# Performance work log

Hardware: AMD Instinct MI355X
Metric: run time of the kernel (lower is better)

## Reference

```python
import jax, jax.numpy as jnp
import numpy as np

N0, N1, N2 = 200000, 50000, 10000
E1, E2 = 800000, 160000
IN_F, HID, RANK, OUT_C = 128, 128, 64, 64


def _cp_graphconv(feat_src, feat_dst, src, dst, n_dst, W_src, W_dst, W_out, b):
    # CP-rank factorized GraphConv: project src feats to rank space, gather along
    # edges, mean-aggregate per dst node, multiply elementwise with dst rank
    # projection (CP / Hadamard fusion), then project to output space.
    h_src = feat_src @ W_src                      # [N_src, R]
    msg = h_src[src]                              # [E, R] gather
    agg = jax.ops.segment_sum(msg, dst, num_segments=n_dst)   # [n_dst, R]
    cnt = jax.ops.segment_sum(jnp.ones((dst.shape[0],), msg.dtype), dst, num_segments=n_dst)
    agg = agg / jnp.maximum(cnt, 1.0)[:, None]    # mean aggregation
    z = agg * (feat_dst @ W_dst)                  # [n_dst, R] CP hadamard
    return z @ W_out + b                          # [n_dst, out]


def setup_inputs() -> dict:
    key = jax.random.key(0)
    ks = jax.random.split(key, 12)
    s1 = 1.0 / np.sqrt(IN_F)
    s2 = 1.0 / np.sqrt(HID)
    sr = 1.0 / np.sqrt(RANK)
    return {
        "x": jax.random.normal(ks[0], (N0, IN_F), jnp.float32),
        "W_src1": jax.random.normal(ks[1], (IN_F, RANK), jnp.float32) * s1,
        "W_dst1": jax.random.normal(ks[2], (IN_F, RANK), jnp.float32) * s1,
        "W_out1": jax.random.normal(ks[3], (RANK, HID), jnp.float32) * sr,
        "b1": jnp.zeros((HID,), jnp.float32),
        "W_src2": jax.random.normal(ks[4], (HID, RANK), jnp.float32) * s2,
        "W_dst2": jax.random.normal(ks[5], (HID, RANK), jnp.float32) * s2,
        "W_out2": jax.random.normal(ks[6], (RANK, OUT_C), jnp.float32) * sr,
        "b2": jnp.zeros((OUT_C,), jnp.float32),
        "src1": jax.random.randint(ks[7], (E1,), 0, N0),
        "dst1": jax.random.randint(ks[8], (E1,), 0, N1),
        "src2": jax.random.randint(ks[9], (E2,), 0, N1),
        "dst2": jax.random.randint(ks[10], (E2,), 0, N2),
        "n_dst1": N1,
        "n_dst2": N2,
    }


def reference(x, W_src1, W_dst1, W_out1, b1, W_src2, W_dst2, W_out2, b2,
              src1, dst1, src2, dst2, n_dst1, n_dst2):
    h_dst = x[:n_dst1]
    h = _cp_graphconv(x, h_dst, src1, dst1, n_dst1, W_src1, W_dst1, W_out1, b1)
    h = jax.nn.relu(h)
    # dropout: eval mode (training=False) -> identity
    h_dst2 = h[:n_dst2]
    out = _cp_graphconv(h, h_dst2, src2, dst2, n_dst2, W_src2, W_dst2, W_out2, b2)
    return out
```

## Files before the change

kernel.cpp:

```cpp
#include <hip/hip_runtime.h>
#include <hip/hip_bf16.h>
#include <hip/hip_fp16.h>

#define N0 200000
#define N1 50000
#define N2 10000
#define E1C 800000
#define E2C 160000
#define NB1 784
#define NB2 160
#define NBT (NB1 + NB2)
#define CH1 64
#define CH2 16
#define NTP 12500
#define NT1 3125
#define NT2 625
#define SCAP 2048

struct H8 { __half2 a, b, c, d; };

typedef _Float16 f16x8 __attribute__((ext_vector_type(8)));
typedef float f32x4 __attribute__((ext_vector_type(4)));
#define MFMA16(a, b, c) __builtin_amdgcn_mfma_f32_16x16x32_f16(a, b, c, 0, 0, 0)

#define WT_TOTAL 45056

__global__ __launch_bounds__(256) void prep_count(const int* __restrict__ dst1,
                                                  const int* __restrict__ dst2,
                                                  int* __restrict__ hist_part,
                                                  const float* __restrict__ Wsrc1,
                                                  const float* __restrict__ Wdst1,
                                                  const float* __restrict__ Wout1,
                                                  const float* __restrict__ Wsrc2,
                                                  const float* __restrict__ Wdst2,
                                                  const float* __restrict__ Wout2,
                                                  __half* __restrict__ wt) {
    int b = blockIdx.x;
    if (b < CH1 + CH2) {
        __shared__ int hl[NB1];
        const int* dst; int nb, e0, n4, hoff;
        if (b < CH1) {
            dst = dst1; nb = NB1; int per = E1C / CH1 / 4; e0 = b * per; n4 = per;
            hoff = b * NB1;
        } else {
            dst = dst2; nb = NB2; int per = E2C / CH2 / 4; int c = b - CH1;
            e0 = c * per; n4 = per;
            hoff = CH1 * NB1 + c * NB2;
        }
        for (int i = threadIdx.x; i < nb; i += 256) hl[i] = 0;
        __syncthreads();
        const int4* d4 = reinterpret_cast<const int4*>(dst);
        for (int i = e0 + threadIdx.x; i < e0 + n4; i += 256) {
            int4 v = d4[i];
            atomicAdd(&hl[v.x >> 6], 1);
            atomicAdd(&hl[v.y >> 6], 1);
            atomicAdd(&hl[v.z >> 6], 1);
            atomicAdd(&hl[v.w >> 6], 1);
        }
        __syncthreads();
        for (int i = threadIdx.x; i < nb; i += 256) hist_part[hoff + i] = hl[i];
    } else {
        int e = (b - (CH1 + CH2)) * 256 + threadIdx.x;
        if (e < WT_TOTAL) {
            float v;
            if (e < 8192)       { int e2 = e;         int n = e2 >> 7, k = e2 & 127; v = Wsrc1[k * 64 + n]; }
            else if (e < 16384) { int e2 = e - 8192;  int n = e2 >> 7, k = e2 & 127; v = Wdst1[k * 64 + n]; }
            else if (e < 24576) { int e2 = e - 16384; int n = e2 >> 6, k = e2 & 63;  v = Wout1[k * 128 + n]; }
            else if (e < 32768) { int e2 = e - 24576; int n = e2 >> 7, k = e2 & 127; v = Wsrc2[k * 64 + n]; }
            else if (e < 40960) { int e2 = e - 32768; int n = e2 >> 7, k = e2 & 127; v = Wdst2[k * 64 + n]; }
            else                { int e2 = e - 40960; int n = e2 >> 6, k = e2 & 63;  v = Wout2[k * 64 + n]; }
            wt[e] = __float2half(v);
        }
    }
}

__global__ __launch_bounds__(1024) void scan_sum(const int* __restrict__ hp,
                                                 int* __restrict__ hist,
                                                 int* __restrict__ base,
                                                 int* __restrict__ cursor) {
    int t = threadIdx.x, lane = t & 63, wid = t >> 6;
    int v = 0;
    if (t < NB1) {
        #pragma unroll 8
        for (int c = 0; c < CH1; ++c) v += hp[c * NB1 + t];
    } else if (t < NBT) {
        const int* hp2 = hp + CH1 * NB1;
        int j = t - NB1;
        #pragma unroll
        for (int c = 0; c < CH2; ++c) v += hp2[c * NB2 + j];
    }
    if (t < NBT) hist[t] = v;
    int s = v;
    #pragma unroll
    for (int o = 1; o < 64; o <<= 1) { int u = __shfl_up(s, o, 64); if (lane >= o) s += u; }
    __shared__ int ws[16];
    if (lane == 63) ws[wid] = s;
    __syncthreads();
    if (wid == 0 && lane < 16) {
        int w = ws[lane];
        #pragma unroll
        for (int o = 1; o < 16; o <<= 1) { int u = __shfl_up(w, o, 64); if (lane >= o) w += u; }
        ws[lane] = w;
    }
    __syncthreads();
    int excl = ((wid == 0) ? 0 : ws[wid - 1]) + (s - v);
    if (t < NBT) { base[t] = excl; cursor[t] = excl; }
}

__global__ __launch_bounds__(256) void sort_scatter(const int* __restrict__ dst1,
                                                    const int* __restrict__ src1,
                                                    const int* __restrict__ dst2,
                                                    const int* __restrict__ src2,
                                                    int* __restrict__ cursor,
                                                    int* __restrict__ edgebuf) {
    __shared__ int cnt_l[98], lbase[98], rsv[98], lcur[98];
    __shared__ int slot[SCAP];
    __shared__ int stot[2];
    int b = blockIdx.x;
    const int* dst; const int* srcp; int goff, bpp, lo, e0, e1;
    if (b < 8 * CH1) {
        dst = dst1; srcp = src1; goff = 0; bpp = NB1 / 8;
        int part = b & 7, chunk = b >> 3;
        lo = part * bpp;
        int per = E1C / CH1 / 4;
        e0 = chunk * per; e1 = e0 + per;
    } else {
        int k = b - 8 * CH1;
        dst = dst2; srcp = src2; goff = NB1; bpp = NB2 / 8;
        int part = k & 7, chunk = k >> 3;
        lo = part * bpp;
        int per = E2C / CH2 / 4;
        e0 = chunk * per; e1 = e0 + per;
    }
    int t = threadIdx.x;
    for (int i = t; i < bpp; i += 256) { cnt_l[i] = 0; lcur[i] = 0; }
    __syncthreads();
    const int4* d4 = reinterpret_cast<const int4*>(dst);
    const int4* s4 = reinterpret_cast<const int4*>(srcp);
    for (int i = e0 + t; i < e1; i += 256) {
        int4 v = d4[i];
        int b0 = (v.x >> 6) - lo; if ((unsigned)b0 < (unsigned)bpp) atomicAdd(&cnt_l[b0], 1);
        int b1 = (v.y >> 6) - lo; if ((unsigned)b1 < (unsigned)bpp) atomicAdd(&cnt_l[b1], 1);
        int b2 = (v.z >> 6) - lo; if ((unsigned)b2 < (unsigned)bpp) atomicAdd(&cnt_l[b2], 1);
        int b3 = (v.w >> 6) - lo; if ((unsigned)b3 < (unsigned)bpp) atomicAdd(&cnt_l[b3], 1);
    }
    __syncthreads();
    if (t < 128) {
        int j = t;
        int lane6 = t & 63;
        int v = (j < bpp) ? cnt_l[j] : 0;
        int s = v;
        #pragma unroll
        for (int o = 1; o < 64; o <<= 1) { int u = __shfl_up(s, o, 64); if (lane6 >= o) s += u; }
        if (lane6 == 63) stot[t >> 6] = s;
        if (j < bpp) lbase[j] = s - v;
    }
    __syncthreads();
    if (t >= 64 && t < 128) {
        int j = t;
        if (j < bpp) lbase[j] += stot[0];
    }
    __syncthreads();
    int T = stot[0] + stot[1];
    if (T <= SCAP) {
        for (int i = e0 + t; i < e1; i += 256) {
            int4 dv = d4[i];
            int4 sv = s4[i];
            int b0 = (dv.x >> 6) - lo;
            if ((unsigned)b0 < (unsigned)bpp) { int p = atomicAdd(&lcur[b0], 1); slot[lbase[b0] + p] = (b0 << 24) | (sv.x << 6) | (dv.x & 63); }
            int b1 = (dv.y >> 6) - lo;
            if ((unsigned)b1 < (unsigned)bpp) { int p = atomicAdd(&lcur[b1], 1); slot[lbase[b1] + p] = (b1 << 24) | (sv.y << 6) | (dv.y & 63); }
            int b2 = (dv.z >> 6) - lo;
            if ((unsigned)b2 < (unsigned)bpp) { int p = atomicAdd(&lcur[b2], 1); slot[lbase[b2] + p] = (b2 << 24) | (sv.z << 6) | (dv.z & 63); }
            int b3 = (dv.w >> 6) - lo;
            if ((unsigned)b3 < (unsigned)bpp) { int p = atomicAdd(&lcur[b3], 1); slot[lbase[b3] + p] = (b3 << 24) | (sv.w << 6) | (dv.w & 63); }
        }
        if (t < bpp) rsv[t] = cnt_l[t] ? atomicAdd(&cursor[goff + lo + t], cnt_l[t]) : 0;
        __syncthreads();
        for (int u = t; u < T; u += 256) {
            int w = slot[u];
            int bx = (unsigned)w >> 24;
            edgebuf[rsv[bx] + (u - lbase[bx])] = w & 0x00FFFFFF;
        }
    } else {
        if (t < bpp) rsv[t] = cnt_l[t] ? atomicAdd(&cursor[goff + lo + t], cnt_l[t]) : 0;
        __syncthreads();
        for (int i = e0 + t; i < e1; i += 256) {
            int4 dv = d4[i];
            int4 sv = s4[i];
            int b0 = (dv.x >> 6) - lo;
            if ((unsigned)b0 < (unsigned)bpp) { int p = atomicAdd(&lcur[b0], 1); edgebuf[rsv[b0] + p] = (sv.x << 6) | (dv.x & 63); }
            int b1 = (dv.y >> 6) - lo;
            if ((unsigned)b1 < (unsigned)bpp) { int p = atomicAdd(&lcur[b1], 1); edgebuf[rsv[b1] + p] = (sv.y << 6) | (dv.y & 63); }
            int b2 = (dv.z >> 6) - lo;
            if ((unsigned)b2 < (unsigned)bpp) { int p = atomicAdd(&lcur[b2], 1); edgebuf[rsv[b2] + p] = (sv.z << 6) | (dv.z & 63); }
            int b3 = (dv.w >> 6) - lo;
            if ((unsigned)b3 < (unsigned)bpp) { int p = atomicAdd(&lcur[b3], 1); edgebuf[rsv[b3] + p] = (sv.w << 6) | (dv.w & 63); }
        }
    }
}

__global__ __launch_bounds__(256) void proj1(const float* __restrict__ x,
                                             const __half* __restrict__ wth,
                                             __half* __restrict__ hsrc,
                                             __half* __restrict__ hdst) {
    int wave = threadIdx.x >> 6, lane = threadIdx.x & 63;
    int tile = blockIdx.x * 4 + wave;
    if (tile >= NTP) return;
    int r0 = tile * 16;
    int m = lane & 15, q = lane >> 4;
    const float* A = x + (size_t)(r0 + m) * 128 + q * 8;
    const _Float16* wt = (const _Float16*)wth;
    const _Float16* Wsrc = wt;
    const _Float16* Wdst = wt + 8192;

    f16x8 a[4];
    #pragma unroll
    for (int kc = 0; kc < 4; ++kc) {
        float4 v0 = *(const float4*)(A + kc * 32);
        float4 v1 = *(const float4*)(A + kc * 32 + 4);
        f16x8 tv;
        tv[0] = (_Float16)v0.x; tv[1] = (_Float16)v0.y; tv[2] = (_Float16)v0.z; tv[3] = (_Float16)v0.w;
        tv[4] = (_Float16)v1.x; tv[5] = (_Float16)v1.y; tv[6] = (_Float16)v1.z; tv[7] = (_Float16)v1.w;
        a[kc] = tv;
    }
    f32x4 accS[4];
    #pragma unroll
    for (int nt = 0; nt < 4; ++nt) accS[nt] = (f32x4)(0.0f);
    #pragma unroll
    for (int kc = 0; kc < 4; ++kc)
        #pragma unroll
        for (int nt = 0; nt < 4; ++nt) {
            f16x8 bb = *(const f16x8*)(Wsrc + (nt * 16 + m) * 128 + kc * 32 + q * 8);
            accS[nt] = MFMA16(a[kc], bb, accS[nt]);
        }
    #pragma unroll
    for (int nt = 0; nt < 4; ++nt)
        #pragma unroll
        for (int i = 0; i < 4; ++i)
            hsrc[(size_t)(r0 + q * 4 + i) * 64 + nt * 16 + m] = __float2half(accS[nt][i]);

    if (tile < NT1) {
        f32x4 accD[4];
        #pragma unroll
        for (int nt = 0; nt < 4; ++nt) accD[nt] = (f32x4)(0.0f);
        #pragma unroll
        for (int kc = 0; kc < 4; ++kc)
            #pragma unroll
            for (int nt = 0; nt < 4; ++nt) {
                f16x8 bb = *(const f16x8*)(Wdst + (nt * 16 + m) * 128 + kc * 32 + q * 8);
                accD[nt] = MFMA16(a[kc], bb, accD[nt]);
            }
        #pragma unroll
        for (int nt = 0; nt < 4; ++nt)
            #pragma unroll
            for (int i = 0; i < 4; ++i)
                hdst[(size_t)(r0 + q * 4 + i) * 64 + nt * 16 + m] = __float2half(accD[nt][i]);
    }
}

__global__ __launch_bounds__(256) void seg1l1(const __half* __restrict__ X,
                                              const __half* __restrict__ hdst1,
                                              const int* __restrict__ edgebuf,
                                              const int* __restrict__ base,
                                              const int* __restrict__ hist,
                                              const __half* __restrict__ wth,
                                              const float* __restrict__ b1,
                                              __half* __restrict__ hsrc2,
                                              __half* __restrict__ hdst2) {
    __shared__ int cnt_lds[64];
    __shared__ int ell[64 * 64];
    __shared__ _Float16 agg[64][72];
    __shared__ _Float16 zt[4][16][136];
    int bkt = blockIdx.x;
    int ebase = base[bkt];
    int ecnt = hist[bkt];
    if (threadIdx.x < 64) cnt_lds[threadIdx.x] = 0;
    __syncthreads();
    for (int i = threadIdx.x; i < ecnt; i += 256) {
        int v = edgebuf[ebase + i];
        int ld = v & 63;
        int p = atomicAdd(&cnt_lds[ld], 1);
        if (p < 64) ell[(ld << 6) + p] = v >> 6;
    }
    __syncthreads();
    int wid = threadIdx.x >> 6, lane = threadIdx.x & 63;
    int sub = lane >> 3, fq = lane & 7;
    const H8* Xr = reinterpret_cast<const H8*>(X);
    for (int ld = wid; ld < 64; ld += 4) {
        int d = (bkt << 6) + ld;
        if (d >= N1) continue;
        int cn = cnt_lds[ld];
        int mm = cn < 64 ? cn : 64;
        float acc[8];
        #pragma unroll
        for (int i = 0; i < 8; ++i) acc[i] = 0.0f;
        for (int e = sub; e < mm; e += 8) {
            int sidx = ell[(ld << 6) + e];
            H8 p = Xr[(size_t)sidx * 8 + fq];
            float2 f0 = __half22float2(p.a);
            float2 f1 = __half22float2(p.b);
            float2 f2 = __half22float2(p.c);
            float2 f3 = __half22float2(p.d);
            acc[0] += f0.x; acc[1] += f0.y; acc[2] += f1.x; acc[3] += f1.y;
            acc[4] += f2.x; acc[5] += f2.y; acc[6] += f3.x; acc[7] += f3.y;
        }
        #pragma unroll
        for (int o = 8; o <= 32; o <<= 1) {
            #pragma unroll
            for (int i = 0; i < 8; ++i) acc[i] += __shfl_xor(acc[i], o, 64);
        }
        if (sub == 0) {
            float inv = (cn > 0) ? (1.0f / (float)cn) : 0.0f;
            H8 o;
            o.a = __floats2half2_rn(acc[0] * inv, acc[1] * inv);
            o.b = __floats2half2_rn(acc[2] * inv, acc[3] * inv);
            o.c = __floats2half2_rn(acc[4] * inv, acc[5] * inv);
            o.d = __floats2half2_rn(acc[6] * inv, acc[7] * inv);
            *reinterpret_cast<H8*>(&agg[ld][fq * 8]) = o;
        }
    }
    __syncthreads();
    int tile = bkt * 4 + wid;
    if (tile >= NT1) return;
    int r0 = tile * 16;
    int m = lane & 15, q = lane >> 4;
    int lm = wid * 16 + m;
    const _Float16* Ad = (const _Float16*)hdst1 + (size_t)(r0 + m) * 64 + q * 8;
    const _Float16* wt = (const _Float16*)wth;
    const _Float16* Wout  = wt + 16384;
    const _Float16* Wsrc2 = wt + 24576;
    const _Float16* Wdst2 = wt + 32768;

    f32x4 acc2[8];
    #pragma unroll
    for (int nt = 0; nt < 8; ++nt) acc2[nt] = (f32x4)(0.0f);
    #pragma unroll
    for (int kc = 0; kc < 2; ++kc) {
        f16x8 az = *(const f16x8*)(&agg[lm][kc * 32 + q * 8]);
        f16x8 ad = *(const f16x8*)(Ad + kc * 32);
        f16x8 z;
        #pragma unroll
        for (int i = 0; i < 8; ++i) z[i] = (_Float16)((float)az[i] * (float)ad[i]);
        #pragma unroll
        for (int nt = 0; nt < 8; ++nt) {
            f16x8 bo = *(const f16x8*)(Wout + (nt * 16 + m) * 64 + kc * 32 + q * 8);
            acc2[nt] = MFMA16(z, bo, acc2[nt]);
        }
    }
    #pragma unroll
    for (int nt = 0; nt < 8; ++nt) {
        float bz = b1[nt * 16 + m];
        #pragma unroll
        for (int i = 0; i < 4; ++i) {
            float v = fmaxf(acc2[nt][i] + bz, 0.0f);
            zt[wid][q * 4 + i][nt * 16 + m] = (_Float16)v;
        }
    }
    f32x4 accS[4], accD[4];
    #pragma unroll
    for (int nt = 0; nt < 4; ++nt) { accS[nt] = (f32x4)(0.0f); accD[nt] = (f32x4)(0.0f); }
    bool do_dst = (tile < NT2);
    #pragma unroll
    for (int kc = 0; kc < 4; ++kc) {
        f16x8 ah = *(const f16x8*)(&zt[wid][m][kc * 32 + q * 8]);
        #pragma unroll
        for (int nt = 0; nt < 4; ++nt) {
            f16x8 bs = *(const f16x8*)(Wsrc2 + (nt * 16 + m) * 128 + kc * 32 + q * 8);
            accS[nt] = MFMA16(ah, bs, accS[nt]);
        }
        if (do_dst) {
            #pragma unroll
            for (int nt = 0; nt < 4; ++nt) {
                f16x8 bd = *(const f16x8*)(Wdst2 + (nt * 16 + m) * 128 + kc * 32 + q * 8);
                accD[nt] = MFMA16(ah, bd, accD[nt]);
            }
        }
    }
    #pragma unroll
    for (int nt = 0; nt < 4; ++nt)
        #pragma unroll
        for (int i = 0; i < 4; ++i)
            hsrc2[(size_t)(r0 + q * 4 + i) * 64 + nt * 16 + m] = __float2half(accS[nt][i]);
    if (do_dst) {
        #pragma unroll
        for (int nt = 0; nt < 4; ++nt)
            #pragma unroll
            for (int i = 0; i < 4; ++i)
                hdst2[(size_t)(r0 + q * 4 + i) * 64 + nt * 16 + m] = __float2half(accD[nt][i]);
    }
}

__global__ __launch_bounds__(256) void seg2l2(const __half* __restrict__ X,
                                              const __half* __restrict__ hdst2,
                                              const int* __restrict__ edgebuf,
                                              const int* __restrict__ base,
                                              const int* __restrict__ hist,
                                              const __half* __restrict__ wth,
                                              const float* __restrict__ b2,
                                              float* __restrict__ out) {
    __shared__ int cnt_lds[64];
    __shared__ int ell[64 * 64];
    __shared__ _Float16 agg[64][72];
    int bkt = blockIdx.x;
    int gb = NB1 + bkt;
    int ebase = base[gb];
    int ecnt = hist[gb];
    if (threadIdx.x < 64) cnt_lds[threadIdx.x] = 0;
    __syncthreads();
    for (int i = threadIdx.x; i < ecnt; i += 256) {
        int v = edgebuf[ebase + i];
        int ld = v & 63;
        int p = atomicAdd(&cnt_lds[ld], 1);
        if (p < 64) ell[(ld << 6) + p] = v >> 6;
    }
    __syncthreads();
    int wid = threadIdx.x >> 6, lane = threadIdx.x & 63;
    int sub = lane >> 3, fq = lane & 7;
    const H8* Xr = reinterpret_cast<const H8*>(X);
    for (int ld = wid; ld < 64; ld += 4) {
        int d = (bkt << 6) + ld;
        if (d >= N2) continue;
        int cn = cnt_lds[ld];
        int mm = cn < 64 ? cn : 64;
        float acc[8];
        #pragma unroll
        for (int i = 0; i < 8; ++i) acc[i] = 0.0f;
        for (int e = sub; e < mm; e += 8) {
            int sidx = ell[(ld << 6) + e];
            H8 p = Xr[(size_t)sidx * 8 + fq];
            float2 f0 = __half22float2(p.a);
            float2 f1 = __half22float2(p.b);
            float2 f2 = __half22float2(p.c);
            float2 f3 = __half22float2(p.d);
            acc[0] += f0.x; acc[1] += f0.y; acc[2] += f1.x; acc[3] += f1.y;
            acc[4] += f2.x; acc[5] += f2.y; acc[6] += f3.x; acc[7] += f3.y;
        }
        #pragma unroll
        for (int o = 8; o <= 32; o <<= 1) {
            #pragma unroll
            for (int i = 0; i < 8; ++i) acc[i] += __shfl_xor(acc[i], o, 64);
        }
        if (sub == 0) {
            float inv = (cn > 0) ? (1.0f / (float)cn) : 0.0f;
            H8 o;
            o.a = __floats2half2_rn(acc[0] * inv, acc[1] * inv);
            o.b = __floats2half2_rn(acc[2] * inv, acc[3] * inv);
            o.c = __floats2half2_rn(acc[4] * inv, acc[5] * inv);
            o.d = __floats2half2_rn(acc[6] * inv, acc[7] * inv);
            *reinterpret_cast<H8*>(&agg[ld][fq * 8]) = o;
        }
    }
    __syncthreads();
    int tile = bkt * 4 + wid;
    if (tile >= NT2) return;
    int r0 = tile * 16;
    int m = lane & 15, q = lane >> 4;
    int lm = wid * 16 + m;
    const _Float16* Ad = (const _Float16*)hdst2 + (size_t)(r0 + m) * 64 + q * 8;
    const _Float16* Wout = (const _Float16*)wth + 40960;

    f32x4 acc[4];
    #pragma unroll
    for (int nt = 0; nt < 4; ++nt) acc[nt] = (f32x4)(0.0f);
    #pragma unroll
    for (int kc = 0; kc < 2; ++kc) {
        f16x8 az = *(const f16x8*)(&agg[lm][kc * 32 + q * 8]);
        f16x8 ad = *(const f16x8*)(Ad + kc * 32);
        f16x8 z;
        #pragma unroll
        for (int i = 0; i < 8; ++i) z[i] = (_Float16)((float)az[i] * (float)ad[i]);
        #pragma unroll
        for (int nt = 0; nt < 4; ++nt) {
            f16x8 bo = *(const f16x8*)(Wout + (nt * 16 + m) * 64 + kc * 32 + q * 8);
            acc[nt] = MFMA16(z, bo, acc[nt]);
        }
    }
    #pragma unroll
    for (int nt = 0; nt < 4; ++nt) {
        float bz = b2[nt * 16 + m];
        #pragma unroll
        for (int i = 0; i < 4; ++i)
            out[(size_t)(r0 + q * 4 + i) * 64 + nt * 16 + m] = acc[nt][i] + bz;
    }
}

extern "C" void kernel_launch(void* const* d_in, const int* in_sizes, int n_in,
                              void* d_out, int out_size, void* d_ws, size_t ws_size,
                              hipStream_t stream) {
    const float* x     = (const float*)d_in[0];
    const float* Wsrc1 = (const float*)d_in[1];
    const float* Wdst1 = (const float*)d_in[2];
    const float* Wout1 = (const float*)d_in[3];
    const float* b1    = (const float*)d_in[4];
    const float* Wsrc2 = (const float*)d_in[5];
    const float* Wdst2 = (const float*)d_in[6];
    const float* Wout2 = (const float*)d_in[7];
    const float* b2    = (const float*)d_in[8];
    const int* src1    = (const int*)d_in[9];
    const int* dst1    = (const int*)d_in[10];
    const int* src2    = (const int*)d_in[11];
    const int* dst2    = (const int*)d_in[12];
    float* out = (float*)d_out;

    char* basep = (char*)d_ws;
    __half* hsrc1 = (__half*)(basep);
    __half* hdst1 = (__half*)(basep + 25600000);
    __half* hsrc2 = (__half*)(basep + 32000000);
    __half* hdst2 = (__half*)(basep + 38400000);
    int* hist     = (int*)(basep + 39680000);
    int* bbase    = (int*)(basep + 39683776);
    int* cursor   = (int*)(basep + 39687552);
    int* histp    = (int*)(basep + 39691328);
    int* edgebuf  = (int*)(basep + 39902272);
    __half* wt    = (__half*)(basep + 43742272);

    prep_count<<<CH1 + CH2 + WT_TOTAL / 256, 256, 0, stream>>>(dst1, dst2, histp,
                                                               Wsrc1, Wdst1, Wout1, Wsrc2, Wdst2, Wout2, wt);
    scan_sum<<<1, 1024, 0, stream>>>(histp, hist, bbase, cursor);
    sort_scatter<<<8 * CH1 + 8 * CH2, 256, 0, stream>>>(dst1, src1, dst2, src2, cursor, edgebuf);
    proj1<<<(NTP + 3) / 4, 256, 0, stream>>>(x, wt, hsrc1, hdst1);
    seg1l1<<<782, 256, 0, stream>>>(hsrc1, hdst1, edgebuf, bbase, hist, wt, b1, hsrc2, hdst2);
    seg2l2<<<157, 256, 0, stream>>>(hsrc2, hdst2, edgebuf, bbase, hist, wt, b2, out);
}
```

Before: 318.9 us.

## Split each 64-node bucket across four blocks and unroll edge gather by two

Each segment-aggregation kernel now launches four blocks per 64-destination bucket, each handling 16 destination nodes and filtering the bucket's edge list to its slice, with one wave doing the follow-up MFMA projections. The aim is more blocks in flight and higher occupancy thanks to smaller LDS use, plus more outstanding gathers from the two-way unrolled edge loop. In exchange, every block rereads the whole bucket's edge list (four times the edgebuf traffic), and three of the four waves sit idle during the matrix phase.

```diff
diff --git a/kernel.cpp b/kernel.cpp
--- a/kernel.cpp
+++ b/kernel.cpp
@@ -268,40 +268,60 @@
                                               const float* __restrict__ b1,
                                               __half* __restrict__ hsrc2,
                                               __half* __restrict__ hdst2) {
-    __shared__ int cnt_lds[64];
-    __shared__ int ell[64 * 64];
-    __shared__ _Float16 agg[64][72];
-    __shared__ _Float16 zt[4][16][136];
-    int bkt = blockIdx.x;
+    __shared__ int cnt_lds[16];
+    __shared__ int ell[16 * 64];
+    __shared__ _Float16 agg[16][72];
+    __shared__ _Float16 zt[16][136];
+    int bkt = blockIdx.x >> 2, s = blockIdx.x & 3;
+    int d0 = (bkt << 6) + (s << 4);
+    if (d0 >= N1) return;
     int ebase = base[bkt];
     int ecnt = hist[bkt];
-    if (threadIdx.x < 64) cnt_lds[threadIdx.x] = 0;
-    __syncthreads();
+    if (threadIdx.x < 16) cnt_lds[threadIdx.x] = 0;
+    __syncthreads();
+    int lo16 = s << 4;
     for (int i = threadIdx.x; i < ecnt; i += 256) {
         int v = edgebuf[ebase + i];
-        int ld = v & 63;
-        int p = atomicAdd(&cnt_lds[ld], 1);
-        if (p < 64) ell[(ld << 6) + p] = v >> 6;
+        int ld = (v & 63) - lo16;
+        if ((unsigned)ld < 16u) {
+            int p = atomicAdd(&cnt_lds[ld], 1);
+            if (p < 64) ell[(ld << 6) + p] = v >> 6;
+        }
     }
     __syncthreads();
     int wid = threadIdx.x >> 6, lane = threadIdx.x & 63;
     int sub = lane >> 3, fq = lane & 7;
     const H8* Xr = reinterpret_cast<const H8*>(X);
-    for (int ld = wid; ld < 64; ld += 4) {
-        int d = (bkt << 6) + ld;
-        if (d >= N1) continue;
+    #pragma unroll
+    for (int j = 0; j < 4; ++j) {
+        int ld = wid * 4 + j;
         int cn = cnt_lds[ld];
         int mm = cn < 64 ? cn : 64;
         float acc[8];
         #pragma unroll
         for (int i = 0; i < 8; ++i) acc[i] = 0.0f;
-        for (int e = sub; e < mm; e += 8) {
-            int sidx = ell[(ld << 6) + e];
-            H8 p = Xr[(size_t)sidx * 8 + fq];
-            float2 f0 = __half22float2(p.a);
-            float2 f1 = __half22float2(p.b);
-            float2 f2 = __half22float2(p.c);
-            float2 f3 = __half22float2(p.d);
+        int e = sub;
+        for (; e + 8 < mm; e += 16) {
+            int s0 = ell[(ld << 6) + e];
+            int s1 = ell[(ld << 6) + e + 8];
+            H8 p0 = Xr[(size_t)s0 * 8 + fq];
+            H8 p1 = Xr[(size_t)s1 * 8 + fq];
+            float2 f0 = __half22float2(p0.a), g0 = __half22float2(p1.a);
+            float2 f1 = __half22float2(p0.b), g1 = __half22float2(p1.b);
+            float2 f2 = __half22float2(p0.c), g2 = __half22float2(p1.c);
+            float2 f3 = __half22float2(p0.d), g3 = __half22float2(p1.d);
+            acc[0] += f0.x + g0.x; acc[1] += f0.y + g0.y;
+            acc[2] += f1.x + g1.x; acc[3] += f1.y + g1.y;
+            acc[4] += f2.x + g2.x; acc[5] += f2.y + g2.y;
+            acc[6] += f3.x + g3.x; acc[7] += f3.y + g3.y;
+        }
+        if (e < mm) {
+            int s0 = ell[(ld << 6) + e];
+            H8 p0 = Xr[(size_t)s0 * 8 + fq];
+            float2 f0 = __half22float2(p0.a);
+            float2 f1 = __half22float2(p0.b);
+            float2 f2 = __half22float2(p0.c);
+            float2 f3 = __half22float2(p0.d);
             acc[0] += f0.x; acc[1] += f0.y; acc[2] += f1.x; acc[3] += f1.y;
             acc[4] += f2.x; acc[5] += f2.y; acc[6] += f3.x; acc[7] += f3.y;
         }
@@ -321,11 +341,10 @@
         }
     }
     __syncthreads();
-    int tile = bkt * 4 + wid;
-    if (tile >= NT1) return;
-    int r0 = tile * 16;
+    if (wid != 0) return;
+    int tile = (bkt << 2) + s;
+    int r0 = d0;
     int m = lane & 15, q = lane >> 4;
-    int lm = wid * 16 + m;
     const _Float16* Ad = (const _Float16*)hdst1 + (size_t)(r0 + m) * 64 + q * 8;
     const _Float16* wt = (const _Float16*)wth;
     const _Float16* Wout  = wt + 16384;
@@ -337,7 +356,7 @@
     for (int nt = 0; nt < 8; ++nt) acc2[nt] = (f32x4)(0.0f);
     #pragma unroll
     for (int kc = 0; kc < 2; ++kc) {
-        f16x8 az = *(const f16x8*)(&agg[lm][kc * 32 + q * 8]);
+        f16x8 az = *(const f16x8*)(&agg[m][kc * 32 + q * 8]);
         f16x8 ad = *(const f16x8*)(Ad + kc * 32);
         f16x8 z;
         #pragma unroll
@@ -354,7 +373,7 @@
         #pragma unroll
         for (int i = 0; i < 4; ++i) {
             float v = fmaxf(acc2[nt][i] + bz, 0.0f);
-            zt[wid][q * 4 + i][nt * 16 + m] = (_Float16)v;
+            zt[q * 4 + i][nt * 16 + m] = (_Float16)v;
         }
     }
     f32x4 accS[4], accD[4];
@@ -363,7 +382,7 @@
     bool do_dst = (tile < NT2);
     #pragma unroll
     for (int kc = 0; kc < 4; ++kc) {
-        f16x8 ah = *(const f16x8*)(&zt[wid][m][kc * 32 + q * 8]);
+        f16x8 ah = *(const f16x8*)(&zt[m][kc * 32 + q * 8]);
         #pragma unroll
         for (int nt = 0; nt < 4; ++nt) {
             f16x8 bs = *(const f16x8*)(Wsrc2 + (nt * 16 + m) * 128 + kc * 32 + q * 8);
@@ -399,40 +418,60 @@
                                               const __half* __restrict__ wth,
                                               const float* __restrict__ b2,
                                               float* __restrict__ out) {
-    __shared__ int cnt_lds[64];
-    __shared__ int ell[64 * 64];
-    __shared__ _Float16 agg[64][72];
-    int bkt = blockIdx.x;
+    __shared__ int cnt_lds[16];
+    __shared__ int ell[16 * 64];
+    __shared__ _Float16 agg[16][72];
+    int bkt = blockIdx.x >> 2, s = blockIdx.x & 3;
+    int d0 = (bkt << 6) + (s << 4);
+    if (d0 >= N2) return;
     int gb = NB1 + bkt;
     int ebase = base[gb];
     int ecnt = hist[gb];
-    if (threadIdx.x < 64) cnt_lds[threadIdx.x] = 0;
-    __syncthreads();
+    if (threadIdx.x < 16) cnt_lds[threadIdx.x] = 0;
+    __syncthreads();
+    int lo16 = s << 4;
     for (int i = threadIdx.x; i < ecnt; i += 256) {
         int v = edgebuf[ebase + i];
-        int ld = v & 63;
-        int p = atomicAdd(&cnt_lds[ld], 1);
-        if (p < 64) ell[(ld << 6) + p] = v >> 6;
+        int ld = (v & 63) - lo16;
+        if ((unsigned)ld < 16u) {
+            int p = atomicAdd(&cnt_lds[ld], 1);
+            if (p < 64) ell[(ld << 6) + p] = v >> 6;
+        }
     }
     __syncthreads();
     int wid = threadIdx.x >> 6, lane = threadIdx.x & 63;
     int sub = lane >> 3, fq = lane & 7;
     const H8* Xr = reinterpret_cast<const H8*>(X);
-    for (int ld = wid; ld < 64; ld += 4) {
-        int d = (bkt << 6) + ld;
-        if (d >= N2) continue;
+    #pragma unroll
+    for (int j = 0; j < 4; ++j) {
+        int ld = wid * 4 + j;
         int cn = cnt_lds[ld];
         int mm = cn < 64 ? cn : 64;
         float acc[8];
         #pragma unroll
         for (int i = 0; i < 8; ++i) acc[i] = 0.0f;
-        for (int e = sub; e < mm; e += 8) {
-            int sidx = ell[(ld << 6) + e];
-            H8 p = Xr[(size_t)sidx * 8 + fq];
-            float2 f0 = __half22float2(p.a);
-            float2 f1 = __half22float2(p.b);
-            float2 f2 = __half22float2(p.c);
-            float2 f3 = __half22float2(p.d);
+        int e = sub;
+        for (; e + 8 < mm; e += 16) {
+            int s0 = ell[(ld << 6) + e];
+            int s1 = ell[(ld << 6) + e + 8];
+            H8 p0 = Xr[(size_t)s0 * 8 + fq];
+            H8 p1 = Xr[(size_t)s1 * 8 + fq];
+            float2 f0 = __half22float2(p0.a), g0 = __half22float2(p1.a);
+            float2 f1 = __half22float2(p0.b), g1 = __half22float2(p1.b);
+            float2 f2 = __half22float2(p0.c), g2 = __half22float2(p1.c);
+            float2 f3 = __half22float2(p0.d), g3 = __half22float2(p1.d);
+            acc[0] += f0.x + g0.x; acc[1] += f0.y + g0.y;
+            acc[2] += f1.x + g1.x; acc[3] += f1.y + g1.y;
+            acc[4] += f2.x + g2.x; acc[5] += f2.y + g2.y;
+            acc[6] += f3.x + g3.x; acc[7] += f3.y + g3.y;
+        }
+        if (e < mm) {
+            int s0 = ell[(ld << 6) + e];
+            H8 p0 = Xr[(size_t)s0 * 8 + fq];
+            float2 f0 = __half22float2(p0.a);
+            float2 f1 = __half22float2(p0.b);
+            float2 f2 = __half22float2(p0.c);
+            float2 f3 = __half22float2(p0.d);
             acc[0] += f0.x; acc[1] += f0.y; acc[2] += f1.x; acc[3] += f1.y;
             acc[4] += f2.x; acc[5] += f2.y; acc[6] += f3.x; acc[7] += f3.y;
         }
@@ -452,11 +491,9 @@
         }
     }
     __syncthreads();
-    int tile = bkt * 4 + wid;
-    if (tile >= NT2) return;
-    int r0 = tile * 16;
+    if (wid != 0) return;
+    int r0 = d0;
     int m = lane & 15, q = lane >> 4;
-    int lm = wid * 16 + m;
     const _Float16* Ad = (const _Float16*)hdst2 + (size_t)(r0 + m) * 64 + q * 8;
     const _Float16* Wout = (const _Float16*)wth + 40960;
 
@@ -465,7 +502,7 @@
     for (int nt = 0; nt < 4; ++nt) acc[nt] = (f32x4)(0.0f);
     #pragma unroll
     for (int kc = 0; kc < 2; ++kc) {
-        f16x8 az = *(const f16x8*)(&agg[lm][kc * 32 + q * 8]);
+        f16x8 az = *(const f16x8*)(&agg[m][kc * 32 + q * 8]);
         f16x8 ad = *(const f16x8*)(Ad + kc * 32);
         f16x8 z;
         #pragma unroll
@@ -520,6 +557,6 @@
     scan_sum<<<1, 1024, 0, stream>>>(histp, hist, bbase, cursor);
     sort_scatter<<<8 * CH1 + 8 * CH2, 256, 0, stream>>>(dst1, src1, dst2, src2, cursor, edgebuf);
     proj1<<<(NTP + 3) / 4, 256, 0, stream>>>(x, wt, hsrc1, hdst1);
-    seg1l1<<<782, 256, 0, stream>>>(hsrc1, hdst1, edgebuf, bbase, hist, wt, b1, hsrc2, hdst2);
-    seg2l2<<<157, 256, 0, stream>>>(hsrc2, hdst2, edgebuf, bbase, hist, wt, b2, out);
-}
+    seg1l1<<<782 * 4, 256, 0, stream>>>(hsrc1, hdst1, edgebuf, bbase, hist, wt, b1, hsrc2, hdst2);
+    seg2l2<<<157 * 4, 256, 0, stream>>>(hsrc2, hdst2, edgebuf, bbase, hist, wt, b2, out);
+}
```

After: 276.1 us. 1.16x faster.
